# Kernel tuning notes

Measured on AMD Instinct MI355X. Metric: run time of the kernel, lower is better.

The kernel has to match this reference:

```python
import jax, jax.numpy as jnp
import numpy as np

NUM_HEADS = 8
HEAD_DIM = 64  # hidden_dim // num_heads = 512 // 8
THRESHOLD = 0.5


def setup_inputs() -> dict:
    key = jax.random.key(0)
    ks = jax.random.split(key, 12)
    B, T, D, Hd = 4, 1024, 512, 512
    s = 0.02
    inp = {
        'x': jax.random.normal(ks[0], (B, T, D), dtype=jnp.float32),
        'Wq': jax.random.normal(ks[1], (D, Hd), dtype=jnp.float32) * s,
        'bq': jnp.zeros((Hd,), jnp.float32),
        'Wk': jax.random.normal(ks[2], (D, Hd), dtype=jnp.float32) * s,
        'bk': jnp.zeros((Hd,), jnp.float32),
        'Wv': jax.random.normal(ks[3], (D, Hd), dtype=jnp.float32) * s,
        'bv': jnp.zeros((Hd,), jnp.float32),
        'conv_w': jax.random.normal(ks[4], (NUM_HEADS,), dtype=jnp.float32) * 0.3,
        'conv_b': jnp.zeros((1,), jnp.float32),
        'Wfh': jax.random.normal(ks[5], (Hd, Hd), dtype=jnp.float32) * s,
        'bfh': jnp.zeros((Hd,), jnp.float32),
        'Wfg': jax.random.normal(ks[6], (Hd, Hd), dtype=jnp.float32) * s,
        'bfg': jnp.zeros((Hd,), jnp.float32),
        'Wrh': jax.random.normal(ks[7], (Hd, Hd), dtype=jnp.float32) * s,
        'brh': jnp.zeros((Hd,), jnp.float32),
        'Wrg': jax.random.normal(ks[8], (Hd, Hd), dtype=jnp.float32) * s,
        'brg': jnp.zeros((Hd,), jnp.float32),
    }
    return inp


def reference(x, Wq, bq, Wk, bk, Wv, bv, conv_w, conv_b,
              Wfh, bfh, Wfg, bfg, Wrh, brh, Wrg, brg):
    B, T, D = x.shape
    H, hd = NUM_HEADS, HEAD_DIM
    scale = hd ** -0.5

    q = (x @ Wq + bq).reshape(B, T, H, hd).transpose(0, 2, 1, 3)  # [B,H,T,hd]
    k = (x @ Wk + bk).reshape(B, T, H, hd).transpose(0, 2, 1, 3)
    v = (x @ Wv + bv).reshape(B, T, H, hd).transpose(0, 2, 1, 3)

    scores = jnp.einsum('bhqd,bhkd->bhqk', q, k) * scale        # [B,H,T,T]
    A_t = jax.nn.softmax(scores, axis=-1)

    # cross-head 1x1 conv: weighted sum over heads -> [B,1,T,T]
    R_f = jax.nn.sigmoid(jnp.einsum('bhqk,h->bqk', A_t, conv_w) + conv_b[0])
    R_f = R_f[:, None]                                           # [B,1,T,T]
    M_f = (R_f <= THRESHOLD).astype(A_t.dtype)
    M_r = (1.0 - R_f <= THRESHOLD).astype(A_t.dtype)

    A_f = jax.nn.softmax(A_t * M_f, axis=-1)
    A_r = jax.nn.softmax(A_t * M_r, axis=-1)

    T_f = jnp.einsum('bhqk,bhkd->bhqd', A_f, v).transpose(0, 2, 1, 3).reshape(B, T, H * hd)
    T_r = jnp.einsum('bhqk,bhkd->bhqd', A_r, v).transpose(0, 2, 1, 3).reshape(B, T, H * hd)

    F_f = T_f @ Wfh + bfh
    G_f = jax.nn.sigmoid(T_f @ Wfg + bfg)
    F_r = T_r @ Wrh + brh
    G_r = jax.nn.sigmoid(T_r @ Wrg + brg)

    G_cat = jax.nn.softmax(jnp.stack([G_f, G_r], axis=-1), axis=-1)  # [B,T,Hd,2]
    F_t = F_f * G_cat[..., 0] + F_r * G_cat[..., 1]
    return F_t
```

## Files before the change

### kernel.cpp

```cpp
#include <hip/hip_runtime.h>
#include <hip/hip_bf16.h>
#include <stdint.h>

typedef short bf16x8 __attribute__((ext_vector_type(8)));
typedef float f32x4 __attribute__((ext_vector_type(4)));

__device__ __forceinline__ unsigned short f2bf(float f) {
  union { float f; unsigned int u; } v;
  v.f = f;
  unsigned int u = v.u;
  u = (u + 0x7fffu + ((u >> 16) & 1u)) >> 16;
  return (unsigned short)u;
}

__device__ __forceinline__ unsigned int pack_bf16(float x, float y) {
  return (unsigned int)f2bf(x) | ((unsigned int)f2bf(y) << 16);
}

typedef union { bf16x8 v; unsigned int u[4]; } frag_u;

__device__ __forceinline__ void gload16(const void* g, void* lds) {
  __builtin_amdgcn_global_load_lds(
      (const __attribute__((address_space(1))) unsigned int*)(unsigned long long)g,
      (__attribute__((address_space(3))) unsigned int*)(unsigned long long)(unsigned)(unsigned long long)lds,
      16, 0, 0);
}

__device__ __forceinline__ bf16x8 lds_frag(const unsigned short* t, int row, int ch4q) {
  return *(const bf16x8*)(t + row * 64 + ((ch4q ^ (row & 7)) << 3));
}


__global__ __launch_bounds__(256) void prep_kernel(
    const float* __restrict__ x,
    const float* __restrict__ Wq, const float* __restrict__ Wk, const float* __restrict__ Wv,
    const float* __restrict__ Wfh, const float* __restrict__ Wfg,
    const float* __restrict__ Wrh, const float* __restrict__ Wrg,
    unsigned short* __restrict__ xb, unsigned short* __restrict__ wt) {
  int bid = blockIdx.x;
  int tid = threadIdx.x;
  if (bid < 448) {
    __shared__ float tile[64][65];
    int mat = bid >> 6;
    int t = bid & 63;
    int tr = (t >> 3) * 64, tc = (t & 7) * 64;
    const float* W = (mat == 0) ? Wq : (mat == 1) ? Wk : (mat == 2) ? Wv
                   : (mat == 3) ? Wfh : (mat == 4) ? Wfg : (mat == 5) ? Wrh : Wrg;
    unsigned short* Wt = wt + (size_t)mat * 512 * 512;
    for (int rep = 0; rep < 16; rep++) {
      int idx = rep * 256 + tid;
      int r = idx >> 6, c = idx & 63;
      tile[r][c] = W[(tr + r) * 512 + tc + c];
    }
    __syncthreads();
    for (int rep = 0; rep < 16; rep++) {
      int idx = rep * 256 + tid;
      int r = idx >> 6, c = idx & 63;
      Wt[(tc + r) * 512 + tr + c] = f2bf(tile[c][r]);
    }
  } else {
    int blk = bid - 448;
    const float4* xi = (const float4*)x;
    for (int rep = 0; rep < 32; rep++) {
      int i = blk * 256 + tid + rep * 16384;
      float4 v = xi[i];
      unsigned int lo = (unsigned int)f2bf(v.x) | ((unsigned int)f2bf(v.y) << 16);
      unsigned int hi = (unsigned int)f2bf(v.z) | ((unsigned int)f2bf(v.w) << 16);
      uint2 u; u.x = lo; u.y = hi;
      *(uint2*)&xb[(size_t)i * 4] = u;
    }
  }
}

__global__ __launch_bounds__(256, 2) void qkv_kernel(
    const unsigned short* __restrict__ xb,
    const unsigned short* __restrict__ wtq, const unsigned short* __restrict__ wtk,
    const unsigned short* __restrict__ wtv,
    const float* __restrict__ bq, const float* __restrict__ bk, const float* __restrict__ bv,
    unsigned short* __restrict__ Qfrag, unsigned short* __restrict__ Kfrag,
    unsigned short* __restrict__ Vfrag) {
  __shared__ unsigned short As[64 * 64];
  __shared__ unsigned short Bq[64 * 64];
  __shared__ unsigned short Bk[64 * 64];
  __shared__ unsigned short Bv[64 * 64];
  __shared__ __attribute__((aligned(16))) unsigned short st[3][64 * 72];
  const int m0 = blockIdx.y * 64, n0 = blockIdx.x * 64;
  const int tid = threadIdx.x, w = tid >> 6, lane = tid & 63;
  const int c = lane & 15, quad = lane >> 4;
  const int wm = w & 1, wn = w >> 1;
  const int rsel = lane >> 3, csel = lane & 7;
  const int sc = csel ^ rsel;
  const char* Ag  = (const char*)xb  + (size_t)(m0 + w * 16 + rsel) * 1024 + sc * 16;
  const char* Bgq = (const char*)wtq + (size_t)(n0 + w * 16 + rsel) * 1024 + sc * 16;
  const char* Bgk = (const char*)wtk + (size_t)(n0 + w * 16 + rsel) * 1024 + sc * 16;
  const char* Bgv = (const char*)wtv + (size_t)(n0 + w * 16 + rsel) * 1024 + sc * 16;
  unsigned short* lA = &As[w * 1024];
  unsigned short* lQ = &Bq[w * 1024];
  unsigned short* lK = &Bk[w * 1024];
  unsigned short* lV = &Bv[w * 1024];

  f32x4 acc[3][2][2];
  f32x4 z4 = {0.f, 0.f, 0.f, 0.f};
#pragma unroll
  for (int o = 0; o < 3; o++)
#pragma unroll
    for (int i = 0; i < 2; i++)
#pragma unroll
      for (int j = 0; j < 2; j++) acc[o][i][j] = z4;

  for (int ks = 0; ks < 8; ks++) {
    if (ks) __syncthreads();
    const int kb = ks * 128;
    gload16(Ag + kb, lA);        gload16(Ag + kb + 8192, lA + 512);
    gload16(Bgq + kb, lQ);       gload16(Bgq + kb + 8192, lQ + 512);
    gload16(Bgk + kb, lK);       gload16(Bgk + kb + 8192, lK + 512);
    gload16(Bgv + kb, lV);       gload16(Bgv + kb + 8192, lV + 512);
    __syncthreads();
#pragma unroll
    for (int ch = 0; ch < 2; ch++) {
      const int cq = ch * 4 + quad;
      bf16x8 a0 = lds_frag(As, wm * 32 + c, cq);
      bf16x8 a1 = lds_frag(As, wm * 32 + 16 + c, cq);
#pragma unroll
      for (int nt = 0; nt < 2; nt++) {
        const int rb = wn * 32 + nt * 16 + c;
        bf16x8 fq = lds_frag(Bq, rb, cq);
        bf16x8 fk = lds_frag(Bk, rb, cq);
        bf16x8 fv = lds_frag(Bv, rb, cq);
        acc[0][0][nt] = __builtin_amdgcn_mfma_f32_16x16x32_bf16(a0, fq, acc[0][0][nt], 0, 0, 0);
        acc[0][1][nt] = __builtin_amdgcn_mfma_f32_16x16x32_bf16(a1, fq, acc[0][1][nt], 0, 0, 0);
        acc[1][0][nt] = __builtin_amdgcn_mfma_f32_16x16x32_bf16(a0, fk, acc[1][0][nt], 0, 0, 0);
        acc[1][1][nt] = __builtin_amdgcn_mfma_f32_16x16x32_bf16(a1, fk, acc[1][1][nt], 0, 0, 0);
        acc[2][0][nt] = __builtin_amdgcn_mfma_f32_16x16x32_bf16(a0, fv, acc[2][0][nt], 0, 0, 0);
        acc[2][1][nt] = __builtin_amdgcn_mfma_f32_16x16x32_bf16(a1, fv, acc[2][1][nt], 0, 0, 0);
      }
    }
  }

#pragma unroll
  for (int ms = 0; ms < 2; ms++)
#pragma unroll
    for (int nt = 0; nt < 2; nt++) {
      int n_l = wn * 32 + nt * 16 + c;
      int n = n0 + n_l;
      float biasq = bq[n], biask = bk[n], biasv = bv[n];
#pragma unroll
      for (int r = 0; r < 4; r++) {
        int m_l = wm * 32 + ms * 16 + quad * 4 + r;
        st[0][m_l * 72 + n_l] = f2bf((acc[0][ms][nt][r] + biasq) * 0.125f);
        st[1][m_l * 72 + n_l] = f2bf(acc[1][ms][nt][r] + biask);
        st[2][n_l * 72 + m_l] = f2bf(acc[2][ms][nt][r] + biasv);
      }
    }
  __syncthreads();

  {
    const int h = n0 >> 6;
    const int bb = m0 >> 10, t0b = (m0 & 1023) >> 4;
#pragma unroll
    for (int sub = 0; sub < 2; sub++) {
      uint4 vq = *(uint4*)&st[0][(w * 16 + c) * 72 + sub * 32 + quad * 8];
      uint4 vk = *(uint4*)&st[1][(w * 16 + c) * 72 + sub * 32 + quad * 8];
      size_t base = (size_t)((bb * 64 + t0b + w) * 8192) + h * 1024 + sub * 512 + lane * 8;
      *(uint4*)&Qfrag[base] = vq;
      *(uint4*)&Kfrag[base] = vk;
    }
    const int ktq = t0b + w;
    const int ktp = ktq >> 1, half = ktq & 1;
#pragma unroll
    for (int dm = 0; dm < 4; dm++) {
      uint2 vv = *(uint2*)&st[2][(dm * 16 + c) * 72 + w * 16 + quad * 4];
      size_t base = (size_t)(bb * 8 + h) * 65536 + (size_t)(ktp * 4 + dm) * 512
                  + lane * 8 + half * 4;
      *(uint2*)&Vfrag[base] = vv;
    }
  }
}

__global__ __launch_bounds__(512, 4) void zpass1_kernel(
    const unsigned short* __restrict__ Qfrag, const unsigned short* __restrict__ Kfrag,
    float* __restrict__ Zpart) {
  const int b = blockIdx.x >> 1, khalf = blockIdx.x & 1;
  const int qt = blockIdx.y;
  const int tid = threadIdx.x, w = tid >> 6, lane = tid & 63;
  const int c = lane & 15, quad = lane >> 4;
  __shared__ float zl[8][16];
  if (tid < 128) ((float*)zl)[tid] = 0.f;
  __syncthreads();

  f32x4 z4 = {0.f, 0.f, 0.f, 0.f};
  const size_t qbase = (size_t)((b * 64 + qt) * 8192) + lane * 8;
  bf16x8 qf[8][2];
#pragma unroll
  for (int h = 0; h < 8; h++) {
    qf[h][0] = *(const bf16x8*)&Qfrag[qbase + h * 1024];
    qf[h][1] = *(const bf16x8*)&Qfrag[qbase + h * 1024 + 512];
  }

  float zp[8] = {0, 0, 0, 0, 0, 0, 0, 0};
  for (int i = 0; i < 4; i++) {
    const int kt = khalf * 32 + w * 4 + i;
    const size_t kbase = (size_t)((b * 64 + kt) * 8192) + lane * 8;
#pragma unroll
    for (int h = 0; h < 8; h++) {
      bf16x8 kf0 = *(const bf16x8*)&Kfrag[kbase + h * 1024];
      bf16x8 kf1 = *(const bf16x8*)&Kfrag[kbase + h * 1024 + 512];
      f32x4 s = __builtin_amdgcn_mfma_f32_16x16x32_bf16(kf0, qf[h][0], z4, 0, 0, 0);
      s = __builtin_amdgcn_mfma_f32_16x16x32_bf16(kf1, qf[h][1], s, 0, 0, 0);
      zp[h] += __expf(s[0]) + __expf(s[1]) + __expf(s[2]) + __expf(s[3]);
    }
  }
#pragma unroll
  for (int h = 0; h < 8; h++) {
    float z = zp[h];
    z += __shfl_xor(z, 16); z += __shfl_xor(z, 32);
    if (quad == 0) atomicAdd(&zl[h][c], z);
  }
  __syncthreads();
  if (tid < 128) {
    int h = tid >> 4, q = tid & 15;
    Zpart[(size_t)((b * 64 + qt) * 8 + h) * 32 + khalf * 16 + q] = zl[h][q];
  }
}

__global__ __launch_bounds__(512, 4) void zpass2_kernel(
    const unsigned short* __restrict__ Qfrag, const unsigned short* __restrict__ Kfrag,
    const float* __restrict__ Zpart,
    const float* __restrict__ conv_w, const float* __restrict__ conv_b,
    unsigned int* __restrict__ Mfrag) {
  const int b = blockIdx.x >> 1, khalf = blockIdx.x & 1;
  const int qt = blockIdx.y;
  const int tid = threadIdx.x, w = tid >> 6, lane = tid & 63;
  const int c = lane & 15;

  f32x4 z4 = {0.f, 0.f, 0.f, 0.f};
  const float cb = conv_b[0];
  float cwz[8];
#pragma unroll
  for (int h = 0; h < 8; h++) {
    const float* zp = &Zpart[(size_t)((b * 64 + qt) * 8 + h) * 32];
    cwz[h] = conv_w[h] / (zp[c] + zp[16 + c]);
  }

  const size_t qbase = (size_t)((b * 64 + qt) * 8192) + lane * 8;
  bf16x8 qf[8][2];
#pragma unroll
  for (int h = 0; h < 8; h++) {
    qf[h][0] = *(const bf16x8*)&Qfrag[qbase + h * 1024];
    qf[h][1] = *(const bf16x8*)&Qfrag[qbase + h * 1024 + 512];
  }

  for (int i = 0; i < 4; i++) {
    const int kt = khalf * 32 + w * 4 + i;
    const size_t kbase = (size_t)((b * 64 + kt) * 8192) + lane * 8;
    f32x4 zc = {cb, cb, cb, cb};
#pragma unroll
    for (int h = 0; h < 8; h++) {
      bf16x8 kf0 = *(const bf16x8*)&Kfrag[kbase + h * 1024];
      bf16x8 kf1 = *(const bf16x8*)&Kfrag[kbase + h * 1024 + 512];
      f32x4 s = __builtin_amdgcn_mfma_f32_16x16x32_bf16(kf0, qf[h][0], z4, 0, 0, 0);
      s = __builtin_amdgcn_mfma_f32_16x16x32_bf16(kf1, qf[h][1], s, 0, 0, 0);
      zc[0] += cwz[h] * __expf(s[0]);
      zc[1] += cwz[h] * __expf(s[1]);
      zc[2] += cwz[h] * __expf(s[2]);
      zc[3] += cwz[h] * __expf(s[3]);
    }
    unsigned int packed = 0;
#pragma unroll
    for (int r = 0; r < 4; r++) {
      unsigned int m = (zc[r] <= 0.f ? 1u : 0u) | (zc[r] >= 0.f ? 2u : 0u);
      packed |= m << (8 * r);
    }
    Mfrag[(size_t)(b * 64 + qt) * 4096 + (kt >> 1) * 128 + lane * 2 + (kt & 1)] = packed;
  }
}

__global__ __launch_bounds__(256, 4) void pv_kernel(
    const unsigned short* __restrict__ Qfrag, const unsigned short* __restrict__ Kfrag,
    const unsigned short* __restrict__ Vfrag,
    const unsigned int* __restrict__ Mfrag, const float* __restrict__ Zpart,
    unsigned short* __restrict__ Tfb, unsigned short* __restrict__ Trb) {
  const int h = blockIdx.x;
  const int b = blockIdx.y >> 5, qb = blockIdx.y & 31;
  const int tid = threadIdx.x, w = tid >> 6, lane = tid & 63;
  const int c = lane & 15, quad = lane >> 4;
  const int qloc = w & 1, kh = w >> 1;
  const int qt = qb * 2 + qloc;

  __shared__ __attribute__((aligned(16))) float red[2][4][256][4];
  __shared__ float zb[2][2][16];

  f32x4 z4 = {0.f, 0.f, 0.f, 0.f};
  const size_t qbase = (size_t)((b * 64 + qt) * 8192) + h * 1024 + lane * 8;
  bf16x8 qf0 = *(const bf16x8*)&Qfrag[qbase];
  bf16x8 qf1 = *(const bf16x8*)&Qfrag[qbase + 512];
  const float* zpp = &Zpart[(size_t)((b * 64 + qt) * 8 + h) * 32];
  const float invZ = 1.0f / (zpp[c] + zpp[16 + c]);
  const size_t mbase = (size_t)(b * 64 + qt) * 4096 + lane * 2;
  const size_t vb0 = (size_t)(b * 8 + h) * 65536 + lane * 8;

  frag_u ones;
  ones.u[0] = 0x3F803F80u; ones.u[1] = 0x3F803F80u;
  ones.u[2] = 0x3F803F80u; ones.u[3] = 0x3F803F80u;

  f32x4 accf[4], accr[4];
#pragma unroll
  for (int i = 0; i < 4; i++) { accf[i] = z4; accr[i] = z4; }
  f32x4 acc_zf = z4, acc_zr = z4;

#pragma unroll 2
  for (int ip = 0; ip < 16; ip++) {
    const int ktp = kh * 16 + ip;
    const int kta = ktp * 2, ktb = kta + 1;
    const size_t kba = (size_t)((b * 64 + kta) * 8192) + h * 1024 + lane * 8;
    const size_t kbb = (size_t)((b * 64 + ktb) * 8192) + h * 1024 + lane * 8;
    bf16x8 ka0 = *(const bf16x8*)&Kfrag[kba];
    bf16x8 ka1 = *(const bf16x8*)&Kfrag[kba + 512];
    bf16x8 kb0 = *(const bf16x8*)&Kfrag[kbb];
    bf16x8 kb1 = *(const bf16x8*)&Kfrag[kbb + 512];
    f32x4 sa = __builtin_amdgcn_mfma_f32_16x16x32_bf16(ka0, qf0, z4, 0, 0, 0);
    sa = __builtin_amdgcn_mfma_f32_16x16x32_bf16(ka1, qf1, sa, 0, 0, 0);
    f32x4 sb = __builtin_amdgcn_mfma_f32_16x16x32_bf16(kb0, qf0, z4, 0, 0, 0);
    sb = __builtin_amdgcn_mfma_f32_16x16x32_bf16(kb1, qf1, sb, 0, 0, 0);
    const uint2 mp = *(const uint2*)&Mfrag[mbase + (size_t)ktp * 128];
    float ea[4], eb[4];
#pragma unroll
    for (int r = 0; r < 4; r++) {
      ea[r] = __expf(__expf(sa[r]) * invZ);
      eb[r] = __expf(__expf(sb[r]) * invZ);
    }
    frag_u pF, pR;
    pF.u[0] = pack_bf16((mp.x & 0x1u) ? ea[0] : 1.f, (mp.x & 0x100u) ? ea[1] : 1.f);
    pF.u[1] = pack_bf16((mp.x & 0x10000u) ? ea[2] : 1.f, (mp.x & 0x1000000u) ? ea[3] : 1.f);
    pF.u[2] = pack_bf16((mp.y & 0x1u) ? eb[0] : 1.f, (mp.y & 0x100u) ? eb[1] : 1.f);
    pF.u[3] = pack_bf16((mp.y & 0x10000u) ? eb[2] : 1.f, (mp.y & 0x1000000u) ? eb[3] : 1.f);
    pR.u[0] = pack_bf16((mp.x & 0x2u) ? ea[0] : 1.f, (mp.x & 0x200u) ? ea[1] : 1.f);
    pR.u[1] = pack_bf16((mp.x & 0x20000u) ? ea[2] : 1.f, (mp.x & 0x2000000u) ? ea[3] : 1.f);
    pR.u[2] = pack_bf16((mp.y & 0x2u) ? eb[0] : 1.f, (mp.y & 0x200u) ? eb[1] : 1.f);
    pR.u[3] = pack_bf16((mp.y & 0x20000u) ? eb[2] : 1.f, (mp.y & 0x2000000u) ? eb[3] : 1.f);
    acc_zf = __builtin_amdgcn_mfma_f32_16x16x32_bf16(ones.v, pF.v, acc_zf, 0, 0, 0);
    acc_zr = __builtin_amdgcn_mfma_f32_16x16x32_bf16(ones.v, pR.v, acc_zr, 0, 0, 0);
#pragma unroll
    for (int dm = 0; dm < 4; dm++) {
      bf16x8 vf = *(const bf16x8*)&Vfrag[vb0 + (size_t)(ktp * 4 + dm) * 512];
      accf[dm] = __builtin_amdgcn_mfma_f32_16x16x32_bf16(vf, pF.v, accf[dm], 0, 0, 0);
      accr[dm] = __builtin_amdgcn_mfma_f32_16x16x32_bf16(vf, pR.v, accr[dm], 0, 0, 0);
    }
  }

  if (kh == 1) {
#pragma unroll
    for (int dm = 0; dm < 4; dm++) *(f32x4*)red[qloc][dm][lane] = accf[dm];
    if (lane < 16) { zb[qloc][0][lane] = acc_zf[0]; zb[qloc][1][lane] = acc_zr[0]; }
  }
  __syncthreads();
  if (kh == 0) {
#pragma unroll
    for (int dm = 0; dm < 4; dm++) accf[dm] += *(f32x4*)red[qloc][dm][lane];
  }
  __syncthreads();
  if (kh == 1) {
#pragma unroll
    for (int dm = 0; dm < 4; dm++) *(f32x4*)red[qloc][dm][lane] = accr[dm];
  }
  __syncthreads();
  uint2 outf[4], outr[4];
  if (kh == 0) {
#pragma unroll
    for (int dm = 0; dm < 4; dm++) accr[dm] += *(f32x4*)red[qloc][dm][lane];
    const float zf = acc_zf[0] + zb[qloc][0][c];
    const float zr = acc_zr[0] + zb[qloc][1][c];
    const float izf = 1.0f / zf, izr = 1.0f / zr;
#pragma unroll
    for (int dm = 0; dm < 4; dm++) {
      outf[dm].x = pack_bf16(accf[dm][0] * izf, accf[dm][1] * izf);
      outf[dm].y = pack_bf16(accf[dm][2] * izf, accf[dm][3] * izf);
      outr[dm].x = pack_bf16(accr[dm][0] * izr, accr[dm][1] * izr);
      outr[dm].y = pack_bf16(accr[dm][2] * izr, accr[dm][3] * izr);
    }
  }
  __syncthreads();
  unsigned short* ts = (unsigned short*)red;
  if (kh == 0) {
    const int qrow = qloc * 16 + c;
#pragma unroll
    for (int dm = 0; dm < 4; dm++) {
      *(uint2*)&ts[qrow * 72 + dm * 16 + quad * 4] = outf[dm];
      *(uint2*)&ts[(32 + qrow) * 72 + dm * 16 + quad * 4] = outr[dm];
    }
  }
  __syncthreads();
  {
    const int row = tid >> 3, seg = tid & 7;
    const size_t g = (size_t)(b * 1024 + qb * 32 + row) * 512 + h * 64 + seg * 8;
    *(uint4*)&Tfb[g] = *(uint4*)&ts[row * 72 + seg * 8];
    *(uint4*)&Trb[g] = *(uint4*)&ts[(32 + row) * 72 + seg * 8];
  }
}

__global__ __launch_bounds__(256, 3) void final_kernel(
    const unsigned short* __restrict__ Tfb, const unsigned short* __restrict__ Trb,
    const unsigned short* __restrict__ wfh, const unsigned short* __restrict__ wfg,
    const unsigned short* __restrict__ wrh, const unsigned short* __restrict__ wrg,
    const float* __restrict__ bfh, const float* __restrict__ bfg,
    const float* __restrict__ brh, const float* __restrict__ brg,
    float* __restrict__ out) {
  __shared__ unsigned short Atf[64 * 64];
  __shared__ unsigned short Atr[64 * 64];
  __shared__ unsigned short Bfh[64 * 64];
  __shared__ unsigned short Bfg[64 * 64];
  __shared__ unsigned short Brh[64 * 64];
  __shared__ unsigned short Brg[64 * 64];
  const int m0 = blockIdx.y * 64, n0 = blockIdx.x * 64;
  const int tid = threadIdx.x, w = tid >> 6, lane = tid & 63;
  const int c = lane & 15, quad = lane >> 4;
  const int wm = w & 1, wn = w >> 1;
  const int rsel = lane >> 3, csel = lane & 7;
  const int sc = csel ^ rsel;
  const char* Agf = (const char*)Tfb + (size_t)(m0 + w * 16 + rsel) * 1024 + sc * 16;
  const char* Agr = (const char*)Trb + (size_t)(m0 + w * 16 + rsel) * 1024 + sc * 16;
  const char* Bg0 = (const char*)wfh + (size_t)(n0 + w * 16 + rsel) * 1024 + sc * 16;
  const char* Bg1 = (const char*)wfg + (size_t)(n0 + w * 16 + rsel) * 1024 + sc * 16;
  const char* Bg2 = (const char*)wrh + (size_t)(n0 + w * 16 + rsel) * 1024 + sc * 16;
  const char* Bg3 = (const char*)wrg + (size_t)(n0 + w * 16 + rsel) * 1024 + sc * 16;
  unsigned short* lAf = &Atf[w * 1024];
  unsigned short* lAr = &Atr[w * 1024];
  unsigned short* l0 = &Bfh[w * 1024];
  unsigned short* l1 = &Bfg[w * 1024];
  unsigned short* l2 = &Brh[w * 1024];
  unsigned short* l3 = &Brg[w * 1024];

  f32x4 acc[4][2][2];
  f32x4 z4 = {0.f, 0.f, 0.f, 0.f};
#pragma unroll
  for (int o = 0; o < 4; o++)
#pragma unroll
    for (int i = 0; i < 2; i++)
#pragma unroll
      for (int j = 0; j < 2; j++) acc[o][i][j] = z4;

  for (int ks = 0; ks < 8; ks++) {
    if (ks) __syncthreads();
    const int kb = ks * 128;
    gload16(Agf + kb, lAf);  gload16(Agf + kb + 8192, lAf + 512);
    gload16(Agr + kb, lAr);  gload16(Agr + kb + 8192, lAr + 512);
    gload16(Bg0 + kb, l0);   gload16(Bg0 + kb + 8192, l0 + 512);
    gload16(Bg1 + kb, l1);   gload16(Bg1 + kb + 8192, l1 + 512);
    gload16(Bg2 + kb, l2);   gload16(Bg2 + kb + 8192, l2 + 512);
    gload16(Bg3 + kb, l3);   gload16(Bg3 + kb + 8192, l3 + 512);
    __syncthreads();
#pragma unroll
    for (int ch = 0; ch < 2; ch++) {
      const int cq = ch * 4 + quad;
      bf16x8 af0 = lds_frag(Atf, wm * 32 + c, cq);
      bf16x8 af1 = lds_frag(Atf, wm * 32 + 16 + c, cq);
      bf16x8 ar0 = lds_frag(Atr, wm * 32 + c, cq);
      bf16x8 ar1 = lds_frag(Atr, wm * 32 + 16 + c, cq);
#pragma unroll
      for (int nt = 0; nt < 2; nt++) {
        const int rb = wn * 32 + nt * 16 + c;
        bf16x8 f0 = lds_frag(Bfh, rb, cq);
        bf16x8 f1 = lds_frag(Bfg, rb, cq);
        bf16x8 f2 = lds_frag(Brh, rb, cq);
        bf16x8 f3 = lds_frag(Brg, rb, cq);
        acc[0][0][nt] = __builtin_amdgcn_mfma_f32_16x16x32_bf16(af0, f0, acc[0][0][nt], 0, 0, 0);
        acc[0][1][nt] = __builtin_amdgcn_mfma_f32_16x16x32_bf16(af1, f0, acc[0][1][nt], 0, 0, 0);
        acc[1][0][nt] = __builtin_amdgcn_mfma_f32_16x16x32_bf16(af0, f1, acc[1][0][nt], 0, 0, 0);
        acc[1][1][nt] = __builtin_amdgcn_mfma_f32_16x16x32_bf16(af1, f1, acc[1][1][nt], 0, 0, 0);
        acc[2][0][nt] = __builtin_amdgcn_mfma_f32_16x16x32_bf16(ar0, f2, acc[2][0][nt], 0, 0, 0);
        acc[2][1][nt] = __builtin_amdgcn_mfma_f32_16x16x32_bf16(ar1, f2, acc[2][1][nt], 0, 0, 0);
        acc[3][0][nt] = __builtin_amdgcn_mfma_f32_16x16x32_bf16(ar0, f3, acc[3][0][nt], 0, 0, 0);
        acc[3][1][nt] = __builtin_amdgcn_mfma_f32_16x16x32_bf16(ar1, f3, acc[3][1][nt], 0, 0, 0);
      }
    }
  }

#pragma unroll
  for (int ms = 0; ms < 2; ms++)
#pragma unroll
    for (int nt = 0; nt < 2; nt++) {
      int n = n0 + wn * 32 + nt * 16 + c;
      float b0 = bfh[n], b1 = bfg[n], b2 = brh[n], b3 = brg[n];
      int t0 = m0 + wm * 32 + ms * 16 + quad * 4;
#pragma unroll
      for (int r = 0; r < 4; r++) {
        int t = t0 + r;
        float Ff = acc[0][ms][nt][r] + b0;
        float Gf = 1.0f / (1.0f + __expf(-(acc[1][ms][nt][r] + b1)));
        float Fr = acc[2][ms][nt][r] + b2;
        float Gr = 1.0f / (1.0f + __expf(-(acc[3][ms][nt][r] + b3)));
        float ef = __expf(Gf), er = __expf(Gr);
        out[(size_t)t * 512 + n] = (Ff * ef + Fr * er) / (ef + er);
      }
    }
}

extern "C" void kernel_launch(void* const* d_in, const int* in_sizes, int n_in,
                              void* d_out, int out_size, void* d_ws, size_t ws_size,
                              hipStream_t stream) {
  const float* x   = (const float*)d_in[0];
  const float* Wq  = (const float*)d_in[1];
  const float* bq  = (const float*)d_in[2];
  const float* Wk  = (const float*)d_in[3];
  const float* bk  = (const float*)d_in[4];
  const float* Wv  = (const float*)d_in[5];
  const float* bv  = (const float*)d_in[6];
  const float* cw  = (const float*)d_in[7];
  const float* cb  = (const float*)d_in[8];
  const float* Wfh = (const float*)d_in[9];
  const float* bfh = (const float*)d_in[10];
  const float* Wfg = (const float*)d_in[11];
  const float* bfg = (const float*)d_in[12];
  const float* Wrh = (const float*)d_in[13];
  const float* brh = (const float*)d_in[14];
  const float* Wrg = (const float*)d_in[15];
  const float* brg = (const float*)d_in[16];

  char* ws = (char*)d_ws;
  const size_t MB = 1024 * 1024;
  unsigned short* xb    = (unsigned short*)(ws + 0 * MB);
  unsigned short* Qfrag = (unsigned short*)(ws + 4 * MB);
  unsigned short* Kfrag = (unsigned short*)(ws + 8 * MB);
  unsigned short* Vfrag = (unsigned short*)(ws + 12 * MB);
  unsigned short* Tfb   = (unsigned short*)(ws + 16 * MB);
  unsigned short* Trb   = (unsigned short*)(ws + 20 * MB);
  unsigned short* wt    = (unsigned short*)(ws + 24 * MB);
  unsigned int*   Mfrag = (unsigned int*)(ws + 28 * MB);
  float*          Zpart = (float*)(ws + 32 * MB);
  const size_t WSZ = 512 * 512;

  prep_kernel<<<512, 256, 0, stream>>>(x, Wq, Wk, Wv, Wfh, Wfg, Wrh, Wrg, xb, wt);
  qkv_kernel<<<dim3(8, 64), 256, 0, stream>>>(xb, wt + 0 * WSZ, wt + 1 * WSZ, wt + 2 * WSZ,
                                              bq, bk, bv, Qfrag, Kfrag, Vfrag);
  zpass1_kernel<<<dim3(8, 64), 512, 0, stream>>>(Qfrag, Kfrag, Zpart);
  zpass2_kernel<<<dim3(8, 64), 512, 0, stream>>>(Qfrag, Kfrag, Zpart, cw, cb, Mfrag);
  pv_kernel<<<dim3(8, 128), 256, 0, stream>>>(Qfrag, Kfrag, Vfrag, Mfrag, Zpart, Tfb, Trb);
  final_kernel<<<dim3(8, 64), 256, 0, stream>>>(Tfb, Trb, wt + 3 * WSZ, wt + 4 * WSZ,
                                                wt + 5 * WSZ, wt + 6 * WSZ,
                                                bfh, bfg, brh, brg, (float*)d_out);
}
```

Before: 206.7 us.

## Split z-passes into key quarters and halve final GEMM M-tile for more blocks

```diff
diff --git a/kernel.cpp b/kernel.cpp
--- a/kernel.cpp
+++ b/kernel.cpp
@@ -177,10 +177,10 @@
   }
 }
 
-__global__ __launch_bounds__(512, 4) void zpass1_kernel(
+__global__ __launch_bounds__(512, 8) void zpass1_kernel(
     const unsigned short* __restrict__ Qfrag, const unsigned short* __restrict__ Kfrag,
     float* __restrict__ Zpart) {
-  const int b = blockIdx.x >> 1, khalf = blockIdx.x & 1;
+  const int b = blockIdx.x >> 2, kq = blockIdx.x & 3;
   const int qt = blockIdx.y;
   const int tid = threadIdx.x, w = tid >> 6, lane = tid & 63;
   const int c = lane & 15, quad = lane >> 4;
@@ -190,89 +190,80 @@
 
   f32x4 z4 = {0.f, 0.f, 0.f, 0.f};
   const size_t qbase = (size_t)((b * 64 + qt) * 8192) + lane * 8;
-  bf16x8 qf[8][2];
-#pragma unroll
+  const int kt0 = kq * 16 + w * 2;
+  const size_t kb0 = (size_t)((b * 64 + kt0) * 8192) + lane * 8;
+
   for (int h = 0; h < 8; h++) {
-    qf[h][0] = *(const bf16x8*)&Qfrag[qbase + h * 1024];
-    qf[h][1] = *(const bf16x8*)&Qfrag[qbase + h * 1024 + 512];
-  }
-
-  float zp[8] = {0, 0, 0, 0, 0, 0, 0, 0};
-  for (int i = 0; i < 4; i++) {
-    const int kt = khalf * 32 + w * 4 + i;
-    const size_t kbase = (size_t)((b * 64 + kt) * 8192) + lane * 8;
-#pragma unroll
-    for (int h = 0; h < 8; h++) {
-      bf16x8 kf0 = *(const bf16x8*)&Kfrag[kbase + h * 1024];
-      bf16x8 kf1 = *(const bf16x8*)&Kfrag[kbase + h * 1024 + 512];
-      f32x4 s = __builtin_amdgcn_mfma_f32_16x16x32_bf16(kf0, qf[h][0], z4, 0, 0, 0);
-      s = __builtin_amdgcn_mfma_f32_16x16x32_bf16(kf1, qf[h][1], s, 0, 0, 0);
-      zp[h] += __expf(s[0]) + __expf(s[1]) + __expf(s[2]) + __expf(s[3]);
-    }
-  }
-#pragma unroll
-  for (int h = 0; h < 8; h++) {
-    float z = zp[h];
-    z += __shfl_xor(z, 16); z += __shfl_xor(z, 32);
-    if (quad == 0) atomicAdd(&zl[h][c], z);
+    bf16x8 qf0 = *(const bf16x8*)&Qfrag[qbase + h * 1024];
+    bf16x8 qf1 = *(const bf16x8*)&Qfrag[qbase + h * 1024 + 512];
+    float zh = 0.f;
+#pragma unroll
+    for (int i = 0; i < 2; i++) {
+      const size_t kb = kb0 + (size_t)i * 8192 + h * 1024;
+      bf16x8 kf0 = *(const bf16x8*)&Kfrag[kb];
+      bf16x8 kf1 = *(const bf16x8*)&Kfrag[kb + 512];
+      f32x4 s = __builtin_amdgcn_mfma_f32_16x16x32_bf16(kf0, qf0, z4, 0, 0, 0);
+      s = __builtin_amdgcn_mfma_f32_16x16x32_bf16(kf1, qf1, s, 0, 0, 0);
+      zh += __expf(s[0]) + __expf(s[1]) + __expf(s[2]) + __expf(s[3]);
+    }
+    zh += __shfl_xor(zh, 16); zh += __shfl_xor(zh, 32);
+    if (quad == 0) atomicAdd(&zl[h][c], zh);
   }
   __syncthreads();
   if (tid < 128) {
     int h = tid >> 4, q = tid & 15;
-    Zpart[(size_t)((b * 64 + qt) * 8 + h) * 32 + khalf * 16 + q] = zl[h][q];
-  }
-}
-
-__global__ __launch_bounds__(512, 4) void zpass2_kernel(
+    Zpart[(size_t)((b * 64 + qt) * 8 + h) * 64 + kq * 16 + q] = zl[h][q];
+  }
+}
+
+__global__ __launch_bounds__(512, 8) void zpass2_kernel(
     const unsigned short* __restrict__ Qfrag, const unsigned short* __restrict__ Kfrag,
     const float* __restrict__ Zpart,
     const float* __restrict__ conv_w, const float* __restrict__ conv_b,
     unsigned int* __restrict__ Mfrag) {
-  const int b = blockIdx.x >> 1, khalf = blockIdx.x & 1;
+  const int b = blockIdx.x >> 2, kq = blockIdx.x & 3;
   const int qt = blockIdx.y;
   const int tid = threadIdx.x, w = tid >> 6, lane = tid & 63;
   const int c = lane & 15;
 
   f32x4 z4 = {0.f, 0.f, 0.f, 0.f};
   const float cb = conv_b[0];
-  float cwz[8];
-#pragma unroll
+  const size_t qbase = (size_t)((b * 64 + qt) * 8192) + lane * 8;
+  const int kt0 = kq * 16 + w * 2;
+  const size_t kb0 = (size_t)((b * 64 + kt0) * 8192) + lane * 8;
+
+  f32x4 zc0 = {cb, cb, cb, cb};
+  f32x4 zc1 = zc0;
+
   for (int h = 0; h < 8; h++) {
-    const float* zp = &Zpart[(size_t)((b * 64 + qt) * 8 + h) * 32];
-    cwz[h] = conv_w[h] / (zp[c] + zp[16 + c]);
-  }
-
-  const size_t qbase = (size_t)((b * 64 + qt) * 8192) + lane * 8;
-  bf16x8 qf[8][2];
-#pragma unroll
-  for (int h = 0; h < 8; h++) {
-    qf[h][0] = *(const bf16x8*)&Qfrag[qbase + h * 1024];
-    qf[h][1] = *(const bf16x8*)&Qfrag[qbase + h * 1024 + 512];
-  }
-
-  for (int i = 0; i < 4; i++) {
-    const int kt = khalf * 32 + w * 4 + i;
-    const size_t kbase = (size_t)((b * 64 + kt) * 8192) + lane * 8;
-    f32x4 zc = {cb, cb, cb, cb};
-#pragma unroll
-    for (int h = 0; h < 8; h++) {
-      bf16x8 kf0 = *(const bf16x8*)&Kfrag[kbase + h * 1024];
-      bf16x8 kf1 = *(const bf16x8*)&Kfrag[kbase + h * 1024 + 512];
-      f32x4 s = __builtin_amdgcn_mfma_f32_16x16x32_bf16(kf0, qf[h][0], z4, 0, 0, 0);
-      s = __builtin_amdgcn_mfma_f32_16x16x32_bf16(kf1, qf[h][1], s, 0, 0, 0);
-      zc[0] += cwz[h] * __expf(s[0]);
-      zc[1] += cwz[h] * __expf(s[1]);
-      zc[2] += cwz[h] * __expf(s[2]);
-      zc[3] += cwz[h] * __expf(s[3]);
-    }
-    unsigned int packed = 0;
-#pragma unroll
-    for (int r = 0; r < 4; r++) {
-      unsigned int m = (zc[r] <= 0.f ? 1u : 0u) | (zc[r] >= 0.f ? 2u : 0u);
-      packed |= m << (8 * r);
-    }
-    Mfrag[(size_t)(b * 64 + qt) * 4096 + (kt >> 1) * 128 + lane * 2 + (kt & 1)] = packed;
-  }
+    bf16x8 qf0 = *(const bf16x8*)&Qfrag[qbase + h * 1024];
+    bf16x8 qf1 = *(const bf16x8*)&Qfrag[qbase + h * 1024 + 512];
+    const float* zp = &Zpart[(size_t)((b * 64 + qt) * 8 + h) * 64];
+    const float cwz = conv_w[h] / (zp[c] + zp[16 + c] + zp[32 + c] + zp[48 + c]);
+    const size_t kba = kb0 + h * 1024;
+    bf16x8 ka0 = *(const bf16x8*)&Kfrag[kba];
+    bf16x8 ka1 = *(const bf16x8*)&Kfrag[kba + 512];
+    bf16x8 kb0f = *(const bf16x8*)&Kfrag[kba + 8192];
+    bf16x8 kb1f = *(const bf16x8*)&Kfrag[kba + 8192 + 512];
+    f32x4 sa = __builtin_amdgcn_mfma_f32_16x16x32_bf16(ka0, qf0, z4, 0, 0, 0);
+    sa = __builtin_amdgcn_mfma_f32_16x16x32_bf16(ka1, qf1, sa, 0, 0, 0);
+    f32x4 sb = __builtin_amdgcn_mfma_f32_16x16x32_bf16(kb0f, qf0, z4, 0, 0, 0);
+    sb = __builtin_amdgcn_mfma_f32_16x16x32_bf16(kb1f, qf1, sb, 0, 0, 0);
+    zc0[0] += cwz * __expf(sa[0]); zc0[1] += cwz * __expf(sa[1]);
+    zc0[2] += cwz * __expf(sa[2]); zc0[3] += cwz * __expf(sa[3]);
+    zc1[0] += cwz * __expf(sb[0]); zc1[1] += cwz * __expf(sb[1]);
+    zc1[2] += cwz * __expf(sb[2]); zc1[3] += cwz * __expf(sb[3]);
+  }
+
+  unsigned int p0 = 0, p1 = 0;
+#pragma unroll
+  for (int r = 0; r < 4; r++) {
+    p0 |= ((zc0[r] <= 0.f ? 1u : 0u) | (zc0[r] >= 0.f ? 2u : 0u)) << (8 * r);
+    p1 |= ((zc1[r] <= 0.f ? 1u : 0u) | (zc1[r] >= 0.f ? 2u : 0u)) << (8 * r);
+  }
+  const int ktp = kq * 8 + w;
+  uint2 mm; mm.x = p0; mm.y = p1;
+  *(uint2*)&Mfrag[(size_t)(b * 64 + qt) * 4096 + (size_t)ktp * 128 + lane * 2] = mm;
 }
 
 __global__ __launch_bounds__(256, 4) void pv_kernel(
@@ -294,8 +285,8 @@
   const size_t qbase = (size_t)((b * 64 + qt) * 8192) + h * 1024 + lane * 8;
   bf16x8 qf0 = *(const bf16x8*)&Qfrag[qbase];
   bf16x8 qf1 = *(const bf16x8*)&Qfrag[qbase + 512];
-  const float* zpp = &Zpart[(size_t)((b * 64 + qt) * 8 + h) * 32];
-  const float invZ = 1.0f / (zpp[c] + zpp[16 + c]);
+  const float* zpp = &Zpart[(size_t)((b * 64 + qt) * 8 + h) * 64];
+  const float invZ = 1.0f / (zpp[c] + zpp[16 + c] + zpp[32 + c] + zpp[48 + c]);
   const size_t mbase = (size_t)(b * 64 + qt) * 4096 + lane * 2;
   const size_t vb0 = (size_t)(b * 8 + h) * 65536 + lane * 8;
 
@@ -398,52 +389,50 @@
   }
 }
 
-__global__ __launch_bounds__(256, 3) void final_kernel(
+__global__ __launch_bounds__(256, 4) void final_kernel(
     const unsigned short* __restrict__ Tfb, const unsigned short* __restrict__ Trb,
     const unsigned short* __restrict__ wfh, const unsigned short* __restrict__ wfg,
     const unsigned short* __restrict__ wrh, const unsigned short* __restrict__ wrg,
     const float* __restrict__ bfh, const float* __restrict__ bfg,
     const float* __restrict__ brh, const float* __restrict__ brg,
     float* __restrict__ out) {
-  __shared__ unsigned short Atf[64 * 64];
-  __shared__ unsigned short Atr[64 * 64];
+  __shared__ unsigned short Atf[32 * 64];
+  __shared__ unsigned short Atr[32 * 64];
   __shared__ unsigned short Bfh[64 * 64];
   __shared__ unsigned short Bfg[64 * 64];
   __shared__ unsigned short Brh[64 * 64];
   __shared__ unsigned short Brg[64 * 64];
-  const int m0 = blockIdx.y * 64, n0 = blockIdx.x * 64;
+  const int m0 = blockIdx.y * 32, n0 = blockIdx.x * 64;
   const int tid = threadIdx.x, w = tid >> 6, lane = tid & 63;
   const int c = lane & 15, quad = lane >> 4;
   const int wm = w & 1, wn = w >> 1;
   const int rsel = lane >> 3, csel = lane & 7;
   const int sc = csel ^ rsel;
-  const char* Agf = (const char*)Tfb + (size_t)(m0 + w * 16 + rsel) * 1024 + sc * 16;
-  const char* Agr = (const char*)Trb + (size_t)(m0 + w * 16 + rsel) * 1024 + sc * 16;
+  const char* Agf = (const char*)Tfb + (size_t)(m0 + w * 8 + rsel) * 1024 + sc * 16;
+  const char* Agr = (const char*)Trb + (size_t)(m0 + w * 8 + rsel) * 1024 + sc * 16;
   const char* Bg0 = (const char*)wfh + (size_t)(n0 + w * 16 + rsel) * 1024 + sc * 16;
   const char* Bg1 = (const char*)wfg + (size_t)(n0 + w * 16 + rsel) * 1024 + sc * 16;
   const char* Bg2 = (const char*)wrh + (size_t)(n0 + w * 16 + rsel) * 1024 + sc * 16;
   const char* Bg3 = (const char*)wrg + (size_t)(n0 + w * 16 + rsel) * 1024 + sc * 16;
-  unsigned short* lAf = &Atf[w * 1024];
-  unsigned short* lAr = &Atr[w * 1024];
+  unsigned short* lAf = &Atf[w * 512];
+  unsigned short* lAr = &Atr[w * 512];
   unsigned short* l0 = &Bfh[w * 1024];
   unsigned short* l1 = &Bfg[w * 1024];
   unsigned short* l2 = &Brh[w * 1024];
   unsigned short* l3 = &Brg[w * 1024];
 
-  f32x4 acc[4][2][2];
+  f32x4 acc[4][2];
   f32x4 z4 = {0.f, 0.f, 0.f, 0.f};
 #pragma unroll
   for (int o = 0; o < 4; o++)
 #pragma unroll
-    for (int i = 0; i < 2; i++)
-#pragma unroll
-      for (int j = 0; j < 2; j++) acc[o][i][j] = z4;
+    for (int j = 0; j < 2; j++) acc[o][j] = z4;
 
   for (int ks = 0; ks < 8; ks++) {
     if (ks) __syncthreads();
     const int kb = ks * 128;
-    gload16(Agf + kb, lAf);  gload16(Agf + kb + 8192, lAf + 512);
-    gload16(Agr + kb, lAr);  gload16(Agr + kb + 8192, lAr + 512);
+    gload16(Agf + kb, lAf);
+    gload16(Agr + kb, lAr);
     gload16(Bg0 + kb, l0);   gload16(Bg0 + kb + 8192, l0 + 512);
     gload16(Bg1 + kb, l1);   gload16(Bg1 + kb + 8192, l1 + 512);
     gload16(Bg2 + kb, l2);   gload16(Bg2 + kb + 8192, l2 + 512);
@@ -452,10 +441,8 @@
 #pragma unroll
     for (int ch = 0; ch < 2; ch++) {
       const int cq = ch * 4 + quad;
-      bf16x8 af0 = lds_frag(Atf, wm * 32 + c, cq);
-      bf16x8 af1 = lds_frag(Atf, wm * 32 + 16 + c, cq);
-      bf16x8 ar0 = lds_frag(Atr, wm * 32 + c, cq);
-      bf16x8 ar1 = lds_frag(Atr, wm * 32 + 16 + c, cq);
+      bf16x8 af = lds_frag(Atf, wm * 16 + c, cq);
+      bf16x8 ar = lds_frag(Atr, wm * 16 + c, cq);
 #pragma unroll
       for (int nt = 0; nt < 2; nt++) {
         const int rb = wn * 32 + nt * 16 + c;
@@ -463,36 +450,30 @@
         bf16x8 f1 = lds_frag(Bfg, rb, cq);
         bf16x8 f2 = lds_frag(Brh, rb, cq);
         bf16x8 f3 = lds_frag(Brg, rb, cq);
-        acc[0][0][nt] = __builtin_amdgcn_mfma_f32_16x16x32_bf16(af0, f0, acc[0][0][nt], 0, 0, 0);
-        acc[0][1][nt] = __builtin_amdgcn_mfma_f32_16x16x32_bf16(af1, f0, acc[0][1][nt], 0, 0, 0);
-        acc[1][0][nt] = __builtin_amdgcn_mfma_f32_16x16x32_bf16(af0, f1, acc[1][0][nt], 0, 0, 0);
-        acc[1][1][nt] = __builtin_amdgcn_mfma_f32_16x16x32_bf16(af1, f1, acc[1][1][nt], 0, 0, 0);
-        acc[2][0][nt] = __builtin_amdgcn_mfma_f32_16x16x32_bf16(ar0, f2, acc[2][0][nt], 0, 0, 0);
-        acc[2][1][nt] = __builtin_amdgcn_mfma_f32_16x16x32_bf16(ar1, f2, acc[2][1][nt], 0, 0, 0);
-        acc[3][0][nt] = __builtin_amdgcn_mfma_f32_16x16x32_bf16(ar0, f3, acc[3][0][nt], 0, 0, 0);
-        acc[3][1][nt] = __builtin_amdgcn_mfma_f32_16x16x32_bf16(ar1, f3, acc[3][1][nt], 0, 0, 0);
+        acc[0][nt] = __builtin_amdgcn_mfma_f32_16x16x32_bf16(af, f0, acc[0][nt], 0, 0, 0);
+        acc[1][nt] = __builtin_amdgcn_mfma_f32_16x16x32_bf16(af, f1, acc[1][nt], 0, 0, 0);
+        acc[2][nt] = __builtin_amdgcn_mfma_f32_16x16x32_bf16(ar, f2, acc[2][nt], 0, 0, 0);
+        acc[3][nt] = __builtin_amdgcn_mfma_f32_16x16x32_bf16(ar, f3, acc[3][nt], 0, 0, 0);
       }
     }
   }
 
 #pragma unroll
-  for (int ms = 0; ms < 2; ms++)
-#pragma unroll
-    for (int nt = 0; nt < 2; nt++) {
-      int n = n0 + wn * 32 + nt * 16 + c;
-      float b0 = bfh[n], b1 = bfg[n], b2 = brh[n], b3 = brg[n];
-      int t0 = m0 + wm * 32 + ms * 16 + quad * 4;
-#pragma unroll
-      for (int r = 0; r < 4; r++) {
-        int t = t0 + r;
-        float Ff = acc[0][ms][nt][r] + b0;
-        float Gf = 1.0f / (1.0f + __expf(-(acc[1][ms][nt][r] + b1)));
-        float Fr = acc[2][ms][nt][r] + b2;
-        float Gr = 1.0f / (1.0f + __expf(-(acc[3][ms][nt][r] + b3)));
-        float ef = __expf(Gf), er = __expf(Gr);
-        out[(size_t)t * 512 + n] = (Ff * ef + Fr * er) / (ef + er);
-      }
-    }
+  for (int nt = 0; nt < 2; nt++) {
+    int n = n0 + wn * 32 + nt * 16 + c;
+    float b0 = bfh[n], b1 = bfg[n], b2 = brh[n], b3 = brg[n];
+    int t0 = m0 + wm * 16 + quad * 4;
+#pragma unroll
+    for (int r = 0; r < 4; r++) {
+      int t = t0 + r;
+      float Ff = acc[0][nt][r] + b0;
+      float Gf = 1.0f / (1.0f + __expf(-(acc[1][nt][r] + b1)));
+      float Fr = acc[2][nt][r] + b2;
+      float Gr = 1.0f / (1.0f + __expf(-(acc[3][nt][r] + b3)));
+      float ef = __expf(Gf), er = __expf(Gr);
+      out[(size_t)t * 512 + n] = (Ff * ef + Fr * er) / (ef + er);
+    }
+  }
 }
 
 extern "C" void kernel_launch(void* const* d_in, const int* in_sizes, int n_in,
@@ -532,10 +513,10 @@
   prep_kernel<<<512, 256, 0, stream>>>(x, Wq, Wk, Wv, Wfh, Wfg, Wrh, Wrg, xb, wt);
   qkv_kernel<<<dim3(8, 64), 256, 0, stream>>>(xb, wt + 0 * WSZ, wt + 1 * WSZ, wt + 2 * WSZ,
                                               bq, bk, bv, Qfrag, Kfrag, Vfrag);
-  zpass1_kernel<<<dim3(8, 64), 512, 0, stream>>>(Qfrag, Kfrag, Zpart);
-  zpass2_kernel<<<dim3(8, 64), 512, 0, stream>>>(Qfrag, Kfrag, Zpart, cw, cb, Mfrag);
+  zpass1_kernel<<<dim3(16, 64), 512, 0, stream>>>(Qfrag, Kfrag, Zpart);
+  zpass2_kernel<<<dim3(16, 64), 512, 0, stream>>>(Qfrag, Kfrag, Zpart, cw, cb, Mfrag);
   pv_kernel<<<dim3(8, 128), 256, 0, stream>>>(Qfrag, Kfrag, Vfrag, Mfrag, Zpart, Tfb, Trb);
-  final_kernel<<<dim3(8, 64), 256, 0, stream>>>(Tfb, Trb, wt + 3 * WSZ, wt + 4 * WSZ,
-                                                wt + 5 * WSZ, wt + 6 * WSZ,
-                                                bfh, bfg, brh, brg, (float*)d_out);
-}
+  final_kernel<<<dim3(8, 128), 256, 0, stream>>>(Tfb, Trb, wt + 3 * WSZ, wt + 4 * WSZ,
+                                                 wt + 5 * WSZ, wt + 6 * WSZ,
+                                                 bfh, bfg, brh, brg, (float*)d_out);
+}
```

Result: faster. 194.2 us (-6.1%).
